# Kernel optimization log

Hardware: AMD Instinct MI355X
Metric: run time of the kernel (lower is better)

## Reference

```python
import jax, jax.numpy as jnp
import numpy as np

B, N, D, NNZ = 8, 8192, 64, 2097152

def setup_inputs() -> dict:
    key = jax.random.key(0)
    k1, k2, k3, k4, k5, k6, k7 = jax.random.split(key, 7)
    return {
        "A_batch": jax.random.randint(k1, (NNZ,), 0, B),
        "A_row": jax.random.randint(k2, (NNZ,), 0, N),
        "A_col": jax.random.randint(k3, (NNZ,), 0, N),
        "A_vals": jax.random.normal(k4, (NNZ,), dtype=jnp.float32),
        "X": jax.random.normal(k5, (B, N, D), dtype=jnp.float32),
        "X_mask": jax.random.randint(k6, (B, N), 0, 2).astype(bool),
        "tarX_mask": jax.random.randint(k7, (B, N), 0, 2).astype(bool),
    }

def reference(A_batch, A_row, A_col, A_vals, X, X_mask, tarX_mask):
    # spmamm(A, 2, X, 1, tarX.mask, 'sum'):
    # out[b,i,:] = sum_j A[b,i,j] * X_filled[b,j,:], masked by tarX_mask.
    X_filled = jnp.where(X_mask[..., None], X, 0.0)          # (B,N,D) masked fill
    msg = A_vals[:, None] * X_filled[A_batch, A_col]          # (NNZ,D) gather + scale
    seg = A_batch * N + A_row                                 # linearized (b,i) target
    out = jax.ops.segment_sum(msg, seg, num_segments=B * N).reshape(B, N, D)
    return jnp.where(tarX_mask[..., None], out, 0.0)
```

## Files before the change

kernel.cpp:

```cpp
#include <hip/hip_runtime.h>

#define NB 8
#define NN 8192
#define ND 64

#define NBKT 512
#define ROWS_PER_BKT 128
#define SUB 4
#define NSLOT (NBKT * SUB)
#define SUBCAP 512
#define BKT_CAP (SUB * SUBCAP)
#define CNT_STRIDE 16
#define SPILLCAP 16384

__global__ void mask_prep_kernel(const void* __restrict__ xm_raw,
                                 const void* __restrict__ tm_raw,
                                 unsigned int* __restrict__ xm_out,
                                 unsigned int* __restrict__ tm_out,
                                 int n) {
    __shared__ int s_is_bytes;
    if (threadIdx.x == 0) s_is_bytes = 0;
    __syncthreads();
    {
        const unsigned int* w = (const unsigned int*)xm_raw;
        if (threadIdx.x < 256 && w[threadIdx.x] > 1u) atomicOr(&s_is_bytes, 1);
    }
    __syncthreads();
    const int idx = blockIdx.x * blockDim.x + threadIdx.x;
    if (idx >= n) return;
    unsigned int xv, tv;
    if (s_is_bytes) {
        xv = ((const unsigned char*)xm_raw)[idx];
        tv = ((const unsigned char*)tm_raw)[idx];
    } else {
        xv = ((const unsigned int*)xm_raw)[idx];
        tv = ((const unsigned int*)tm_raw)[idx];
    }
    xm_out[idx] = xv ? 1u : 0u;
    tm_out[idx] = tv ? 1u : 0u;
}

__global__ void bin_kernel(const int* __restrict__ Ab, const int* __restrict__ Ar,
                           const int* __restrict__ Ac, const float* __restrict__ Av,
                           const unsigned int* __restrict__ Xm,
                           const unsigned int* __restrict__ Tm,
                           unsigned int* __restrict__ cnt,
                           int2* __restrict__ buckets,
                           unsigned int* __restrict__ spill_cnt,
                           int2* __restrict__ spill,
                           int nq) {
    const int sub = blockIdx.x & (SUB - 1);
    const int4*   Ab4 = (const int4*)Ab;
    const int4*   Ar4 = (const int4*)Ar;
    const int4*   Ac4 = (const int4*)Ac;
    const float4* Av4 = (const float4*)Av;
    int i = blockIdx.x * blockDim.x + threadIdx.x;
    const int str = gridDim.x * blockDim.x;
    for (; i < nq; i += str) {
        const int4   b4 = Ab4[i];
        const int4   r4 = Ar4[i];
        const int4   c4 = Ac4[i];
        const float4 v4 = Av4[i];
        const int   bs[4] = {b4.x, b4.y, b4.z, b4.w};
        const int   rs[4] = {r4.x, r4.y, r4.z, r4.w};
        const int   cs[4] = {c4.x, c4.y, c4.z, c4.w};
        const float vs[4] = {v4.x, v4.y, v4.z, v4.w};
        #pragma unroll
        for (int j = 0; j < 4; ++j) {
            const int seg  = bs[j] * NN + rs[j];
            const int xrow = bs[j] * NN + cs[j];
            if (Tm[seg] && Xm[xrow]) {
                const int slot = (seg >> 7) * SUB + sub;
                const unsigned int pos = atomicAdd(&cnt[slot * CNT_STRIDE], 1u);
                if (pos < SUBCAP) {
                    buckets[(size_t)slot * SUBCAP + pos] =
                        make_int2(xrow | ((seg & (ROWS_PER_BKT - 1)) << 16),
                                  __float_as_int(vs[j]));
                } else {
                    const unsigned int sp = atomicAdd(spill_cnt, 1u);
                    if (sp < SPILLCAP)
                        spill[sp] = make_int2(xrow | (seg << 16), __float_as_int(vs[j]));
                }
            }
        }
    }
}

__global__ __launch_bounds__(1024) void accum_kernel(const unsigned int* __restrict__ cnt,
                                                     const int2* __restrict__ buckets,
                                                     const float* __restrict__ X,
                                                     float* __restrict__ out) {
    __shared__ int2 sorted[BKT_CAP];
    __shared__ unsigned int hist[ROWS_PER_BKT];
    __shared__ unsigned int rowstart[ROWS_PER_BKT + 1];
    __shared__ unsigned int cursor[ROWS_PER_BKT];
    __shared__ unsigned int s_n[SUB];

    const int bkt = blockIdx.x;
    const int t = threadIdx.x;

    if (t < ROWS_PER_BKT) hist[t] = 0;
    if (t < SUB) s_n[t] = min(cnt[(bkt * SUB + t) * CNT_STRIDE], (unsigned int)SUBCAP);
    __syncthreads();

    int2 e0, e1;
    int r0 = -1, r1 = -1;
    {
        int idx = t, sub = idx >> 9, off = idx & (SUBCAP - 1);
        if ((unsigned int)off < s_n[sub]) {
            e0 = buckets[(size_t)(bkt * SUB + sub) * SUBCAP + off];
            r0 = (e0.x >> 16) & (ROWS_PER_BKT - 1);
            atomicAdd(&hist[r0], 1u);
        }
        idx = t + 1024; sub = idx >> 9; off = idx & (SUBCAP - 1);
        if ((unsigned int)off < s_n[sub]) {
            e1 = buckets[(size_t)(bkt * SUB + sub) * SUBCAP + off];
            r1 = (e1.x >> 16) & (ROWS_PER_BKT - 1);
            atomicAdd(&hist[r1], 1u);
        }
    }
    __syncthreads();

    if (t < 64) {
        const unsigned int h0 = hist[t], h1 = hist[64 + t];
        unsigned int a = h0, b = h1;
        for (int off = 1; off < 64; off <<= 1) {
            unsigned int v = __shfl_up(a, off);
            if (t >= off) a += v;
        }
        const unsigned int atot = __shfl(a, 63);
        for (int off = 1; off < 64; off <<= 1) {
            unsigned int v = __shfl_up(b, off);
            if (t >= off) b += v;
        }
        rowstart[t]      = a - h0;
        rowstart[64 + t] = atot + b - h1;
        cursor[t]        = a - h0;
        cursor[64 + t]   = atot + b - h1;
        if (t == 63) rowstart[128] = atot + b;
    }
    __syncthreads();

    if (r0 >= 0) { const unsigned int p = atomicAdd(&cursor[r0], 1u); sorted[p] = e0; }
    if (r1 >= 0) { const unsigned int p = atomicAdd(&cursor[r1], 1u); sorted[p] = e1; }
    __syncthreads();

    const int wave = t >> 6;
    const int lane = t & 63;
    const int rbase = wave * 8;
    float acc[8];
    #pragma unroll
    for (int j = 0; j < 8; ++j) acc[j] = 0.f;
    #pragma unroll
    for (int j = 0; j < 8; ++j) {
        const unsigned int ks = rowstart[rbase + j];
        const unsigned int ke = rowstart[rbase + j + 1];
        for (unsigned int k = ks; k < ke; ++k) {
            const int2 en = sorted[k];
            acc[j] = fmaf(__int_as_float(en.y),
                          X[((size_t)(en.x & 0xFFFF) << 6) + lane], acc[j]);
        }
    }
    float* obase = out + ((size_t)bkt * ROWS_PER_BKT + rbase) * ND + lane;
    #pragma unroll
    for (int j = 0; j < 8; ++j) obase[(size_t)j * ND] = acc[j];
}

__global__ void spill_kernel(const unsigned int* __restrict__ spill_cnt,
                             const int2* __restrict__ spill,
                             const float* __restrict__ X,
                             float* __restrict__ out) {
    const unsigned int n = min(*spill_cnt, (unsigned int)SPILLCAP);
    const int lane = threadIdx.x & 63;
    const int g0   = blockIdx.x * (blockDim.x >> 6) + (threadIdx.x >> 6);
    const int gstr = gridDim.x * (blockDim.x >> 6);
    for (unsigned int k = g0; k < n; k += gstr) {
        const int2 e   = spill[k];
        const int xrow = e.x & 0xFFFF;
        const int seg  = (e.x >> 16) & 0xFFFF;
        atomicAdd(&out[((size_t)seg << 6) + lane],
                  __int_as_float(e.y) * X[((size_t)xrow << 6) + lane]);
    }
}

__global__ void coo_scatter_kernel(const int* __restrict__ Ab,
                                   const int* __restrict__ Ar,
                                   const int* __restrict__ Ac,
                                   const float* __restrict__ Av,
                                   const float* __restrict__ X,
                                   const unsigned int* __restrict__ Xm,
                                   const unsigned int* __restrict__ Tm,
                                   float* __restrict__ out, int nnz) {
    const int groups_per_block = blockDim.x >> 6;
    const int g0 = blockIdx.x * groups_per_block + (threadIdx.x >> 6);
    const int gstr = gridDim.x * groups_per_block;
    const int lane = threadIdx.x & 63;
    for (int e = g0; e < nnz; e += gstr) {
        const int b = Ab[e];
        const int r = Ar[e];
        if (!Tm[b * NN + r]) continue;
        const int c = Ac[e];
        if (!Xm[b * NN + c]) continue;
        const float v = Av[e];
        const float x = X[((size_t)(b * NN + c)) * ND + lane];
        atomicAdd(&out[((size_t)(b * NN + r)) * ND + lane], v * x);
    }
}

extern "C" void kernel_launch(void* const* d_in, const int* in_sizes, int n_in,
                              void* d_out, int out_size, void* d_ws, size_t ws_size,
                              hipStream_t stream) {
    const int*   Ab = (const int*)d_in[0];
    const int*   Ar = (const int*)d_in[1];
    const int*   Ac = (const int*)d_in[2];
    const float* Av = (const float*)d_in[3];
    const float* X  = (const float*)d_in[4];
    const void*  Xm_raw = d_in[5];
    const void*  Tm_raw = d_in[6];
    float* out = (float*)d_out;

    const int nnz   = in_sizes[0];
    const int nmask = in_sizes[5];

    unsigned char* w = (unsigned char*)d_ws;
    unsigned int* xm        = (unsigned int*)w;  w += (size_t)nmask * 4;
    unsigned int* tm        = (unsigned int*)w;  w += (size_t)nmask * 4;
    unsigned int* cnt       = (unsigned int*)w;  w += (size_t)NSLOT * CNT_STRIDE * 4;
    unsigned int* spill_cnt = (unsigned int*)w;  w += 16;
    int2*         buckets   = (int2*)w;          w += (size_t)NSLOT * SUBCAP * 8;
    int2*         spill     = (int2*)w;          w += (size_t)SPILLCAP * 8;
    const size_t needed = (size_t)(w - (unsigned char*)d_ws);

    mask_prep_kernel<<<(nmask + 255) / 256, 256, 0, stream>>>(Xm_raw, Tm_raw, xm, tm, nmask);

    if (ws_size < needed || nmask != NBKT * ROWS_PER_BKT || (nnz & 3) || nnz > (1 << 22)) {
        hipMemsetAsync(d_out, 0, (size_t)out_size * sizeof(float), stream);
        coo_scatter_kernel<<<16384, 256, 0, stream>>>(Ab, Ar, Ac, Av, X, xm, tm, out, nnz);
        return;
    }

    hipMemsetAsync(cnt, 0, (size_t)NSLOT * CNT_STRIDE * 4 + 16, stream);

    const int nq = nnz >> 2;
    bin_kernel<<<2048, 256, 0, stream>>>(Ab, Ar, Ac, Av, xm, tm,
                                         cnt, buckets, spill_cnt, spill, nq);
    accum_kernel<<<NBKT, 1024, 0, stream>>>(cnt, buckets, X, out);
    spill_kernel<<<16, 256, 0, stream>>>(spill_cnt, spill, X, out);
}
```

Baseline: 174.9 us.

## Fuse mask prep into binning, fold spill into accum, unroll gather loop

Removes the separate mask_prep kernel by detecting the mask element width inside each block of bin_kernel and reading the raw masks directly. Folds the spill handling into accum_kernel, where each wave scans the spill list for its own rows, so the spill kernel and its global atomics go away. It also unrolls the per-row gather-FMA loop by four to issue more independent X loads. The aim is fewer launches and less mask-conversion traffic, at the cost of a per-block detection step and a serial spill scan in every accum block when spills occur.

New measurement: 152.2 us. 13.0% less time.

```diff
diff --git a/kernel.cpp b/kernel.cpp
--- a/kernel.cpp
+++ b/kernel.cpp
@@ -13,42 +13,33 @@
 #define CNT_STRIDE 16
 #define SPILLCAP 16384
 
-__global__ void mask_prep_kernel(const void* __restrict__ xm_raw,
-                                 const void* __restrict__ tm_raw,
-                                 unsigned int* __restrict__ xm_out,
-                                 unsigned int* __restrict__ tm_out,
-                                 int n) {
-    __shared__ int s_is_bytes;
-    if (threadIdx.x == 0) s_is_bytes = 0;
-    __syncthreads();
-    {
-        const unsigned int* w = (const unsigned int*)xm_raw;
-        if (threadIdx.x < 256 && w[threadIdx.x] > 1u) atomicOr(&s_is_bytes, 1);
-    }
-    __syncthreads();
-    const int idx = blockIdx.x * blockDim.x + threadIdx.x;
-    if (idx >= n) return;
-    unsigned int xv, tv;
-    if (s_is_bytes) {
-        xv = ((const unsigned char*)xm_raw)[idx];
-        tv = ((const unsigned char*)tm_raw)[idx];
-    } else {
-        xv = ((const unsigned int*)xm_raw)[idx];
-        tv = ((const unsigned int*)tm_raw)[idx];
-    }
-    xm_out[idx] = xv ? 1u : 0u;
-    tm_out[idx] = tv ? 1u : 0u;
+__device__ __forceinline__ bool detect_bytes_block(const void* xm_raw,
+                                                   int* s_flag) {
+    if (threadIdx.x == 0) *s_flag = 0;
+    __syncthreads();
+    const unsigned int* w = (const unsigned int*)xm_raw;
+    if (threadIdx.x < 256 && w[threadIdx.x] > 1u) atomicOr(s_flag, 1);
+    __syncthreads();
+    return *s_flag != 0;
+}
+
+__device__ __forceinline__ unsigned int mask_at(const void* m, bool bytes, int i) {
+    return bytes ? (unsigned int)((const unsigned char*)m)[i]
+                 : ((const unsigned int*)m)[i];
 }
 
 __global__ void bin_kernel(const int* __restrict__ Ab, const int* __restrict__ Ar,
                            const int* __restrict__ Ac, const float* __restrict__ Av,
-                           const unsigned int* __restrict__ Xm,
-                           const unsigned int* __restrict__ Tm,
+                           const void* __restrict__ Xm_raw,
+                           const void* __restrict__ Tm_raw,
                            unsigned int* __restrict__ cnt,
                            int2* __restrict__ buckets,
                            unsigned int* __restrict__ spill_cnt,
                            int2* __restrict__ spill,
                            int nq) {
+    __shared__ int s_flag;
+    const bool bytes = detect_bytes_block(Xm_raw, &s_flag);
+
     const int sub = blockIdx.x & (SUB - 1);
     const int4*   Ab4 = (const int4*)Ab;
     const int4*   Ar4 = (const int4*)Ar;
@@ -69,7 +60,7 @@
         for (int j = 0; j < 4; ++j) {
             const int seg  = bs[j] * NN + rs[j];
             const int xrow = bs[j] * NN + cs[j];
-            if (Tm[seg] && Xm[xrow]) {
+            if (mask_at(Tm_raw, bytes, seg) && mask_at(Xm_raw, bytes, xrow)) {
                 const int slot = (seg >> 7) * SUB + sub;
                 const unsigned int pos = atomicAdd(&cnt[slot * CNT_STRIDE], 1u);
                 if (pos < SUBCAP) {
@@ -89,33 +80,37 @@
 __global__ __launch_bounds__(1024) void accum_kernel(const unsigned int* __restrict__ cnt,
                                                      const int2* __restrict__ buckets,
                                                      const float* __restrict__ X,
+                                                     const unsigned int* __restrict__ spill_cnt,
+                                                     const int2* __restrict__ spill,
                                                      float* __restrict__ out) {
     __shared__ int2 sorted[BKT_CAP];
     __shared__ unsigned int hist[ROWS_PER_BKT];
     __shared__ unsigned int rowstart[ROWS_PER_BKT + 1];
     __shared__ unsigned int cursor[ROWS_PER_BKT];
     __shared__ unsigned int s_n[SUB];
+    __shared__ unsigned int s_nsp;
 
     const int bkt = blockIdx.x;
     const int t = threadIdx.x;
 
     if (t < ROWS_PER_BKT) hist[t] = 0;
     if (t < SUB) s_n[t] = min(cnt[(bkt * SUB + t) * CNT_STRIDE], (unsigned int)SUBCAP);
-    __syncthreads();
-
-    int2 e0, e1;
+    if (t == 0) s_nsp = min(*spill_cnt, (unsigned int)SPILLCAP);
+    __syncthreads();
+
+    int2 e0s, e1s;
     int r0 = -1, r1 = -1;
     {
         int idx = t, sub = idx >> 9, off = idx & (SUBCAP - 1);
         if ((unsigned int)off < s_n[sub]) {
-            e0 = buckets[(size_t)(bkt * SUB + sub) * SUBCAP + off];
-            r0 = (e0.x >> 16) & (ROWS_PER_BKT - 1);
+            e0s = buckets[(size_t)(bkt * SUB + sub) * SUBCAP + off];
+            r0 = (e0s.x >> 16) & (ROWS_PER_BKT - 1);
             atomicAdd(&hist[r0], 1u);
         }
         idx = t + 1024; sub = idx >> 9; off = idx & (SUBCAP - 1);
         if ((unsigned int)off < s_n[sub]) {
-            e1 = buckets[(size_t)(bkt * SUB + sub) * SUBCAP + off];
-            r1 = (e1.x >> 16) & (ROWS_PER_BKT - 1);
+            e1s = buckets[(size_t)(bkt * SUB + sub) * SUBCAP + off];
+            r1 = (e1s.x >> 16) & (ROWS_PER_BKT - 1);
             atomicAdd(&hist[r1], 1u);
         }
     }
@@ -141,8 +136,8 @@
     }
     __syncthreads();
 
-    if (r0 >= 0) { const unsigned int p = atomicAdd(&cursor[r0], 1u); sorted[p] = e0; }
-    if (r1 >= 0) { const unsigned int p = atomicAdd(&cursor[r1], 1u); sorted[p] = e1; }
+    if (r0 >= 0) { const unsigned int p = atomicAdd(&cursor[r0], 1u); sorted[p] = e0s; }
+    if (r1 >= 0) { const unsigned int p = atomicAdd(&cursor[r1], 1u); sorted[p] = e1s; }
     __syncthreads();
 
     const int wave = t >> 6;
@@ -150,37 +145,47 @@
     const int rbase = wave * 8;
     float acc[8];
     #pragma unroll
-    for (int j = 0; j < 8; ++j) acc[j] = 0.f;
-    #pragma unroll
     for (int j = 0; j < 8; ++j) {
-        const unsigned int ks = rowstart[rbase + j];
+        unsigned int k = rowstart[rbase + j];
         const unsigned int ke = rowstart[rbase + j + 1];
-        for (unsigned int k = ks; k < ke; ++k) {
-            const int2 en = sorted[k];
-            acc[j] = fmaf(__int_as_float(en.y),
-                          X[((size_t)(en.x & 0xFFFF) << 6) + lane], acc[j]);
-        }
-    }
+        float a = 0.f;
+        for (; k + 4 <= ke; k += 4) {
+            const int2 e0 = sorted[k],     e1 = sorted[k + 1];
+            const int2 e2 = sorted[k + 2], e3 = sorted[k + 3];
+            const float x0 = X[((size_t)(e0.x & 0xFFFF) << 6) + lane];
+            const float x1 = X[((size_t)(e1.x & 0xFFFF) << 6) + lane];
+            const float x2 = X[((size_t)(e2.x & 0xFFFF) << 6) + lane];
+            const float x3 = X[((size_t)(e3.x & 0xFFFF) << 6) + lane];
+            a = fmaf(__int_as_float(e0.y), x0, a);
+            a = fmaf(__int_as_float(e1.y), x1, a);
+            a = fmaf(__int_as_float(e2.y), x2, a);
+            a = fmaf(__int_as_float(e3.y), x3, a);
+        }
+        for (; k < ke; ++k) {
+            const int2 e = sorted[k];
+            a = fmaf(__int_as_float(e.y), X[((size_t)(e.x & 0xFFFF) << 6) + lane], a);
+        }
+        acc[j] = a;
+    }
+
+    if (s_nsp) {
+        const int seglo = bkt * ROWS_PER_BKT;
+        for (unsigned int k = 0; k < s_nsp; ++k) {
+            const int2 e = spill[k];
+            const int r = ((e.x >> 16) & 0xFFFF) - seglo;
+            if (r >= rbase && r < rbase + 8) {
+                const float xv = X[((size_t)(e.x & 0xFFFF) << 6) + lane];
+                const float vv = __int_as_float(e.y);
+                #pragma unroll
+                for (int j = 0; j < 8; ++j)
+                    if (r == rbase + j) acc[j] = fmaf(vv, xv, acc[j]);
+            }
+        }
+    }
+
     float* obase = out + ((size_t)bkt * ROWS_PER_BKT + rbase) * ND + lane;
     #pragma unroll
     for (int j = 0; j < 8; ++j) obase[(size_t)j * ND] = acc[j];
-}
-
-__global__ void spill_kernel(const unsigned int* __restrict__ spill_cnt,
-                             const int2* __restrict__ spill,
-                             const float* __restrict__ X,
-                             float* __restrict__ out) {
-    const unsigned int n = min(*spill_cnt, (unsigned int)SPILLCAP);
-    const int lane = threadIdx.x & 63;
-    const int g0   = blockIdx.x * (blockDim.x >> 6) + (threadIdx.x >> 6);
-    const int gstr = gridDim.x * (blockDim.x >> 6);
-    for (unsigned int k = g0; k < n; k += gstr) {
-        const int2 e   = spill[k];
-        const int xrow = e.x & 0xFFFF;
-        const int seg  = (e.x >> 16) & 0xFFFF;
-        atomicAdd(&out[((size_t)seg << 6) + lane],
-                  __int_as_float(e.y) * X[((size_t)xrow << 6) + lane]);
-    }
 }
 
 __global__ void coo_scatter_kernel(const int* __restrict__ Ab,
@@ -188,9 +193,11 @@
                                    const int* __restrict__ Ac,
                                    const float* __restrict__ Av,
                                    const float* __restrict__ X,
-                                   const unsigned int* __restrict__ Xm,
-                                   const unsigned int* __restrict__ Tm,
+                                   const void* __restrict__ Xm_raw,
+                                   const void* __restrict__ Tm_raw,
                                    float* __restrict__ out, int nnz) {
+    __shared__ int s_flag;
+    const bool bytes = detect_bytes_block(Xm_raw, &s_flag);
     const int groups_per_block = blockDim.x >> 6;
     const int g0 = blockIdx.x * groups_per_block + (threadIdx.x >> 6);
     const int gstr = gridDim.x * groups_per_block;
@@ -198,9 +205,9 @@
     for (int e = g0; e < nnz; e += gstr) {
         const int b = Ab[e];
         const int r = Ar[e];
-        if (!Tm[b * NN + r]) continue;
+        if (!mask_at(Tm_raw, bytes, b * NN + r)) continue;
         const int c = Ac[e];
-        if (!Xm[b * NN + c]) continue;
+        if (!mask_at(Xm_raw, bytes, b * NN + c)) continue;
         const float v = Av[e];
         const float x = X[((size_t)(b * NN + c)) * ND + lane];
         atomicAdd(&out[((size_t)(b * NN + r)) * ND + lane], v * x);
@@ -223,27 +230,23 @@
     const int nmask = in_sizes[5];
 
     unsigned char* w = (unsigned char*)d_ws;
-    unsigned int* xm        = (unsigned int*)w;  w += (size_t)nmask * 4;
-    unsigned int* tm        = (unsigned int*)w;  w += (size_t)nmask * 4;
     unsigned int* cnt       = (unsigned int*)w;  w += (size_t)NSLOT * CNT_STRIDE * 4;
     unsigned int* spill_cnt = (unsigned int*)w;  w += 16;
     int2*         buckets   = (int2*)w;          w += (size_t)NSLOT * SUBCAP * 8;
     int2*         spill     = (int2*)w;          w += (size_t)SPILLCAP * 8;
     const size_t needed = (size_t)(w - (unsigned char*)d_ws);
 
-    mask_prep_kernel<<<(nmask + 255) / 256, 256, 0, stream>>>(Xm_raw, Tm_raw, xm, tm, nmask);
-
     if (ws_size < needed || nmask != NBKT * ROWS_PER_BKT || (nnz & 3) || nnz > (1 << 22)) {
         hipMemsetAsync(d_out, 0, (size_t)out_size * sizeof(float), stream);
-        coo_scatter_kernel<<<16384, 256, 0, stream>>>(Ab, Ar, Ac, Av, X, xm, tm, out, nnz);
+        coo_scatter_kernel<<<16384, 256, 0, stream>>>(Ab, Ar, Ac, Av, X,
+                                                      Xm_raw, Tm_raw, out, nnz);
         return;
     }
 
     hipMemsetAsync(cnt, 0, (size_t)NSLOT * CNT_STRIDE * 4 + 16, stream);
 
     const int nq = nnz >> 2;
-    bin_kernel<<<2048, 256, 0, stream>>>(Ab, Ar, Ac, Av, xm, tm,
+    bin_kernel<<<2048, 256, 0, stream>>>(Ab, Ar, Ac, Av, Xm_raw, Tm_raw,
                                          cnt, buckets, spill_cnt, spill, nq);
-    accum_kernel<<<NBKT, 1024, 0, stream>>>(cnt, buckets, X, out);
-    spill_kernel<<<16, 256, 0, stream>>>(spill_cnt, spill, X, out);
-}
+    accum_kernel<<<NBKT, 1024, 0, stream>>>(cnt, buckets, X, spill_cnt, spill, out);
+}
```
